# Optimization experiments

Measured on AMD Instinct MI355X. Metric: run time of the kernel, lower is better.

## Reference

```python
import jax, jax.numpy as jnp
import numpy as np

B, T, C, NH = 4, 2048, 1024, 16
HD = C // NH  # head dim = 64


def setup_inputs() -> dict:
    key = jax.random.key(0)
    ks = jax.random.split(key, 5)
    s = 0.02
    return {
        "x": jax.random.normal(ks[0], (B, T, C), dtype=jnp.float32),
        "W_attn": jax.random.normal(ks[1], (C, 3 * C), dtype=jnp.float32) * s,
        "b_attn": jnp.zeros((3 * C,), dtype=jnp.float32),
        "W_proj": jax.random.normal(ks[2], (C, C), dtype=jnp.float32) * s,
        "b_proj": jnp.zeros((C,), dtype=jnp.float32),
    }


def reference(x, W_attn, b_attn, W_proj, b_proj):
    Bv, Tv, Cv = x.shape
    qkv = x @ W_attn + b_attn  # [B,T,3C]
    q, k, v = jnp.split(qkv, 3, axis=2)
    # [B,T,C] -> [B,NH,T,HD]
    def heads(t):
        return t.reshape(Bv, Tv, NH, HD).transpose(0, 2, 1, 3)
    q, k, v = heads(q), heads(k), heads(v)
    scores = jnp.einsum("bhqd,bhkd->bhqk", q, k) / jnp.sqrt(jnp.float32(HD))
    causal = jnp.tril(jnp.ones((Tv, Tv), dtype=bool))
    scores = jnp.where(causal[None, None, :, :], scores, jnp.float32(-jnp.inf))
    probs = jax.nn.softmax(scores, axis=-1)
    # dropout rate is 0.0 -> identity
    y = jnp.einsum("bhqk,bhkd->bhqd", probs, v)
    y = y.transpose(0, 2, 1, 3).reshape(Bv, Tv, Cv)
    return y @ W_proj + b_proj
```

## Files before the change

kernel.cpp:

```cpp
#include <hip/hip_runtime.h>
#include <hip/hip_bf16.h>

#define Bsz 4
#define Tseq 2048
#define Cdim 1024
#define NH 16
#define HD 64
#define Mrows (Bsz*Tseq)
#define N3C (3*Cdim)

typedef __attribute__((ext_vector_type(8))) short short8;
typedef __attribute__((ext_vector_type(4))) short short4v;
typedef __attribute__((ext_vector_type(4))) float float4v;

__device__ __forceinline__ unsigned short f2b(float f) {
    union { float f; unsigned u; } x; x.f = f;
    unsigned u = x.u;
    u += 0x7fff + ((u >> 16) & 1);
    return (unsigned short)(u >> 16);
}

__device__ __forceinline__ unsigned pk2bf(float a, float b) {
#if __has_builtin(__builtin_amdgcn_cvt_pk_bf16_f32)
    auto w = __builtin_amdgcn_cvt_pk_bf16_f32(a, b);
    unsigned u; __builtin_memcpy(&u, &w, 4);
    return u;
#else
    return (unsigned)f2b(a) | ((unsigned)f2b(b) << 16);
#endif
}

#define GLDS(gp, lp) __builtin_amdgcn_global_load_lds(                         \
    (const __attribute__((address_space(1))) unsigned*)(gp),                   \
    (__attribute__((address_space(3))) unsigned*)(lp), 16, 0, 0)

__global__ __launch_bounds__(256) void cast_kernel(const float* __restrict__ in,
                                                   unsigned short* __restrict__ out, int n) {
    int i = (blockIdx.x * 256 + threadIdx.x) * 4;
    if (i < n) {
        float4 v = *reinterpret_cast<const float4*>(in + i);
        ushort4 o;
        o.x = f2b(v.x); o.y = f2b(v.y); o.z = f2b(v.z); o.w = f2b(v.w);
        *reinterpret_cast<ushort4*>(out + i) = o;
    }
}

__global__ __launch_bounds__(256) void transpose_cast(const float* __restrict__ in,
                                                      unsigned short* __restrict__ out,
                                                      int K, int N) {
    __shared__ float tile[32][33];
    int n0 = blockIdx.x * 32, k0 = blockIdx.y * 32;
    int tx = threadIdx.x & 31, ty = threadIdx.x >> 5;
    #pragma unroll
    for (int i = 0; i < 32; i += 8)
        tile[ty + i][tx] = in[(k0 + ty + i) * N + n0 + tx];
    __syncthreads();
    #pragma unroll
    for (int i = 0; i < 32; i += 8)
        out[(size_t)(n0 + ty + i) * K + k0 + tx] = f2b(tile[tx][ty + i]);
}


#define GROW(r) ((r) * 64 + ((r) >> 3) * 8)

template<bool QKV, int NCOL>
__global__ __launch_bounds__(256) void gemm_bt(const unsigned short* __restrict__ A,
                                               const unsigned short* __restrict__ Bt,
                                               const float* __restrict__ bias,
                                               unsigned short* __restrict__ qb,
                                               unsigned short* __restrict__ kb,
                                               unsigned short* __restrict__ vb,
                                               float* __restrict__ out) {
    __shared__ unsigned short As[8320];
    __shared__ unsigned short Bs[8320];
    int tid = threadIdx.x;
    int lane = tid & 63, wave = tid >> 6;
    int wm = wave >> 1, wn = wave & 1;
    int l15 = lane & 15, quad = lane >> 4;

    int f = blockIdx.x;
    int xcd = f & 7, slot = f >> 3;
    int rowblk = xcd * 8 + (slot & 7);
    int colblk = slot >> 3;
    int row0 = rowblk * 128;
    int col0 = colblk * 128;

    const unsigned short* Ag = A + (size_t)(row0 + wave * 32 + (lane >> 3)) * Cdim + (lane & 7) * 8;
    const unsigned short* Bg = Bt + (size_t)(col0 + wave * 32 + (lane >> 3)) * Cdim + (lane & 7) * 8;
    unsigned short* Al = &As[wave * 2080];
    unsigned short* Bl = &Bs[wave * 2080];

    float4v acc[4][4] = {};

    for (int k0 = 0; k0 < Cdim; k0 += 64) {
        __syncthreads();
        #pragma unroll
        for (int c = 0; c < 4; c++) {
            GLDS(Ag + k0 + (size_t)(c * 8) * Cdim, Al + c * 520);
            GLDS(Bg + k0 + (size_t)(c * 8) * Cdim, Bl + c * 520);
        }
        __syncthreads();

        #pragma unroll
        for (int g = 0; g < 2; g++) {
            short8 af[4], bf[4];
            #pragma unroll
            for (int mi = 0; mi < 4; mi++)
                af[mi] = *(const short8*)&As[GROW(wm * 64 + mi * 16 + l15) + g * 32 + quad * 8];
            #pragma unroll
            for (int ni = 0; ni < 4; ni++)
                bf[ni] = *(const short8*)&Bs[GROW(wn * 64 + ni * 16 + l15) + g * 32 + quad * 8];
            #pragma unroll
            for (int mi = 0; mi < 4; mi++)
                #pragma unroll
                for (int ni = 0; ni < 4; ni++)
                    acc[mi][ni] = __builtin_amdgcn_mfma_f32_16x16x32_bf16(af[mi], bf[ni], acc[mi][ni], 0, 0, 0);
        }
    }

    #pragma unroll
    for (int mi = 0; mi < 4; mi++) {
        #pragma unroll
        for (int ni = 0; ni < 4; ni++) {
            int colb = col0 + wn * 64 + ni * 16 + l15;
            int rowb = row0 + wm * 64 + mi * 16 + quad * 4;
            if (QKV) {
                int p = colb >> 10;
                int h = (colb & 1023) >> 6;
                int d = colb & 63;
                int b = rowb >> 11;
                int t = rowb & 2047;
                if (p == 2) {
                    ushort4 pk;
                    pk.x = f2b(acc[mi][ni][0] + bias[colb]);
                    pk.y = f2b(acc[mi][ni][1] + bias[colb]);
                    pk.z = f2b(acc[mi][ni][2] + bias[colb]);
                    pk.w = f2b(acc[mi][ni][3] + bias[colb]);
                    *(ushort4*)&vb[((size_t)(b * NH + h) * HD + d) * Tseq + t] = pk;
                } else {
                    unsigned short* dst = (p == 0) ? qb : kb;
                    #pragma unroll
                    for (int r = 0; r < 4; r++)
                        dst[((size_t)(b * NH + h) * Tseq + (t + r)) * HD + d] =
                            f2b(acc[mi][ni][r] + bias[colb]);
                }
            } else {
                #pragma unroll
                for (int r = 0; r < 4; r++)
                    out[(size_t)(rowb + r) * Cdim + colb] = acc[mi][ni][r] + bias[colb];
            }
        }
    }
}


__global__ __launch_bounds__(128, 3) void attn_kernel(const unsigned short* __restrict__ qb,
                                                      const unsigned short* __restrict__ kb,
                                                      const unsigned short* __restrict__ vt,
                                                      unsigned short* __restrict__ yb) {
    __shared__ unsigned short Ks[2][64 * 64];
    __shared__ unsigned short Vs[2][64 * 64];

    int tid = threadIdx.x;
    int lane = tid & 63, wave = tid >> 6;
    int l15 = lane & 15, quad = lane >> 4;
    int bh = blockIdx.x;
    int qt = 31 - blockIdx.y;

    const unsigned short* Qh = qb + (size_t)bh * Tseq * HD;
    const unsigned short* Kh = kb + (size_t)bh * Tseq * HD;
    const unsigned short* Vh = vt + (size_t)bh * HD * Tseq;
    int b = bh >> 4, h = bh & 15;
    const float cexp = 0.18033688011112042f;

    int q0 = qt * 64;
    int rb0 = q0 + wave * 32;

    short8 qf[2][2];
    #pragma unroll
    for (int mi = 0; mi < 2; mi++)
        #pragma unroll
        for (int g = 0; g < 2; g++)
            qf[mi][g] = *(const short8*)(Qh + (size_t)(rb0 + mi * 16 + l15) * HD + g * 32 + quad * 8);

    int srow = lane >> 3;
    int scol = ((lane & 7) ^ srow) * 8;
    int sx = l15 & 7;
    int kx0 = ((0 * 4 + quad) ^ sx) * 8;
    int kx1 = ((1 * 4 + quad) ^ sx) * 8;
    int qh_ = quad >> 1, ql_ = quad & 1;

    float4v ov[2][4] = {};
    float m[2]  = {-1e30f, -1e30f};
    float lp[2] = {0.f, 0.f};

    for (int j0 = 0; j0 <= q0; j0 += 128) {
        __syncthreads();
        {
            int jb = j0 + wave * 64;
            const unsigned short* Kg = Kh + (size_t)(jb + srow) * HD + scol;
            const unsigned short* Vg = Vh + (size_t)srow * Tseq + jb + scol;
            unsigned short* Kl = &Ks[wave][0];
            unsigned short* Vl = &Vs[wave][0];
            #pragma unroll
            for (int cc = 0; cc < 8; cc++) {
                GLDS(Kg + (size_t)(cc * 8) * HD, Kl + cc * 512);
                GLDS(Vg + (size_t)(cc * 8) * Tseq, Vl + cc * 512);
            }
        }
        __syncthreads();

        int nh = (j0 + 64 <= q0) ? 2 : 1;
        #pragma unroll 1
        for (int hh = 0; hh < nh; hh++) {
            int j0h = j0 + hh * 64;
            const unsigned short* Kl = &Ks[hh][0];
            const unsigned short* Vl = &Vs[hh][0];

            float4v st[2][4];
            #pragma unroll
            for (int mi = 0; mi < 2; mi++)
                #pragma unroll
                for (int kg = 0; kg < 4; kg++)
                    st[mi][kg] = (float4v){0.f, 0.f, 0.f, 0.f};
            #pragma unroll
            for (int kg = 0; kg < 4; kg++) {
                int krow = kg * 1024 + l15 * 64;
                short8 kf0 = *(const short8*)&Kl[krow + kx0];
                short8 kf1 = *(const short8*)&Kl[krow + kx1];
                st[0][kg] = __builtin_amdgcn_mfma_f32_16x16x32_bf16(kf0, qf[0][0], st[0][kg], 0, 0, 0);
                st[0][kg] = __builtin_amdgcn_mfma_f32_16x16x32_bf16(kf1, qf[0][1], st[0][kg], 0, 0, 0);
                st[1][kg] = __builtin_amdgcn_mfma_f32_16x16x32_bf16(kf0, qf[1][0], st[1][kg], 0, 0, 0);
                st[1][kg] = __builtin_amdgcn_mfma_f32_16x16x32_bf16(kf1, qf[1][1], st[1][kg], 0, 0, 0);
            }

            if (j0h == q0) {
                #pragma unroll
                for (int mi = 0; mi < 2; mi++) {
                    int qrow = rb0 + mi * 16 + l15;
                    #pragma unroll
                    for (int kg = 0; kg < 4; kg++) {
                        int keyb = j0h + kg * 16 + quad * 4;
                        #pragma unroll
                        for (int r = 0; r < 4; r++)
                            if (keyb + r > qrow) st[mi][kg][r] = -1e30f;
                    }
                }
            }

            short4v pf[2][4];
            #pragma unroll
            for (int mi = 0; mi < 2; mi++) {
                float mx = st[mi][0][0];
                #pragma unroll
                for (int kg = 0; kg < 4; kg++)
                    #pragma unroll
                    for (int r = 0; r < 4; r++)
                        mx = fmaxf(mx, st[mi][kg][r]);
                mx = fmaxf(mx, __shfl_xor(mx, 16));
                mx = fmaxf(mx, __shfl_xor(mx, 32));
                float mn = fmaxf(m[mi], mx);
                if (__any(mn > m[mi])) {
                    float alv = __builtin_amdgcn_exp2f((m[mi] - mn) * cexp);
                    m[mi] = mn;
                    lp[mi] *= alv;
                    float ar_[4];
                    #pragma unroll
                    for (int r = 0; r < 4; r++)
                        ar_[r] = __shfl(alv, quad * 4 + r);
                    #pragma unroll
                    for (int dg = 0; dg < 4; dg++)
                        #pragma unroll
                        for (int r = 0; r < 4; r++)
                            ov[mi][dg][r] *= ar_[r];
                }
                float mc = -m[mi] * cexp;
                float sum = 0.f;
                #pragma unroll
                for (int kg = 0; kg < 4; kg++) {
                    float p0 = __builtin_amdgcn_exp2f(__builtin_fmaf(st[mi][kg][0], cexp, mc));
                    float p1 = __builtin_amdgcn_exp2f(__builtin_fmaf(st[mi][kg][1], cexp, mc));
                    float p2 = __builtin_amdgcn_exp2f(__builtin_fmaf(st[mi][kg][2], cexp, mc));
                    float p3 = __builtin_amdgcn_exp2f(__builtin_fmaf(st[mi][kg][3], cexp, mc));
                    sum += (p0 + p1) + (p2 + p3);
                    union { unsigned u[2]; short4v s; } pk_;
                    pk_.u[0] = pk2bf(p0, p1);
                    pk_.u[1] = pk2bf(p2, p3);
                    pf[mi][kg] = pk_.s;
                }
                lp[mi] += sum;
            }

            #pragma unroll
            for (int kg = 0; kg < 4; kg++) {
                int vx = (((kg * 2 + qh_) ^ sx) << 3) + ql_ * 4;
                #pragma unroll
                for (int dg = 0; dg < 4; dg++) {
                    short4v vf = *(const short4v*)&Vl[dg * 1024 + l15 * 64 + vx];
                    ov[0][dg] = __builtin_amdgcn_mfma_f32_16x16x16bf16_1k(pf[0][kg], vf, ov[0][dg], 0, 0, 0);
                    ov[1][dg] = __builtin_amdgcn_mfma_f32_16x16x16bf16_1k(pf[1][kg], vf, ov[1][dg], 0, 0, 0);
                }
            }
        }
    }

    #pragma unroll
    for (int mi = 0; mi < 2; mi++) {
        float lf = lp[mi];
        lf += __shfl_xor(lf, 16);
        lf += __shfl_xor(lf, 32);
        float rinv[4];
        #pragma unroll
        for (int r = 0; r < 4; r++)
            rinv[r] = 1.0f / __shfl(lf, quad * 4 + r);
        #pragma unroll
        for (int dg = 0; dg < 4; dg++)
            #pragma unroll
            for (int r = 0; r < 4; r++) {
                int t = rb0 + mi * 16 + quad * 4 + r;
                yb[((size_t)b * Tseq + t) * Cdim + h * HD + dg * 16 + l15] =
                    f2b(ov[mi][dg][r] * rinv[r]);
            }
    }
}

extern "C" void kernel_launch(void* const* d_in, const int* in_sizes, int n_in,
                              void* d_out, int out_size, void* d_ws, size_t ws_size,
                              hipStream_t stream) {
    const float* x  = (const float*)d_in[0];
    const float* Wa = (const float*)d_in[1];
    const float* ba = (const float*)d_in[2];
    const float* Wp = (const float*)d_in[3];
    const float* bp = (const float*)d_in[4];
    float* out = (float*)d_out;

    unsigned short* ws = (unsigned short*)d_ws;
    unsigned short* xb  = ws;
    unsigned short* Wat = xb  + (size_t)Mrows * Cdim;
    unsigned short* Wpt = Wat + (size_t)N3C * Cdim;
    unsigned short* qb  = Wpt + (size_t)Cdim * Cdim;
    unsigned short* kb  = qb  + (size_t)Bsz * NH * Tseq * HD;
    unsigned short* vb  = kb  + (size_t)Bsz * NH * Tseq * HD;
    unsigned short* yb  = vb  + (size_t)Bsz * NH * Tseq * HD;

    int nx = Mrows * Cdim;
    cast_kernel<<<nx / 4 / 256, 256, 0, stream>>>(x, xb, nx);
    transpose_cast<<<dim3(N3C / 32, Cdim / 32), 256, 0, stream>>>(Wa, Wat, Cdim, N3C);
    transpose_cast<<<dim3(Cdim / 32, Cdim / 32), 256, 0, stream>>>(Wp, Wpt, Cdim, Cdim);

    gemm_bt<true, 24><<<64 * 24, 256, 0, stream>>>(
        xb, Wat, ba, qb, kb, vb, nullptr);

    attn_kernel<<<dim3(Bsz * NH, 32), 128, 0, stream>>>(qb, kb, vb, yb);

    gemm_bt<false, 8><<<64 * 8, 256, 0, stream>>>(
        yb, Wpt, bp, nullptr, nullptr, nullptr, out);
}
```

Measured before the change: 292.7 us.

## Restructure attention into 4-wave blocks with double-buffered K/V prefetch and lazy rescale

The attention kernel moves from 2-wave blocks handling 64 query rows to 4-wave blocks handling 128 query rows, so each K/V tile staged in LDS is shared by twice as many query rows. K/V loading becomes a double-buffered pipeline: the next 64-key tile is prefetched while the current one is computed, with one barrier per iteration. Waves skip key tiles lying fully beyond their causal range. Online-softmax rescaling now happens only when the running max grows by more than a threshold, which cuts rescale work but lets unnormalised exponentials reach larger magnitudes.

```diff
diff --git a/kernel.cpp b/kernel.cpp
--- a/kernel.cpp
+++ b/kernel.cpp
@@ -154,7 +154,7 @@
 }
 
 
-__global__ __launch_bounds__(128, 3) void attn_kernel(const unsigned short* __restrict__ qb,
+__global__ __launch_bounds__(256, 4) void attn_kernel(const unsigned short* __restrict__ qb,
                                                       const unsigned short* __restrict__ kb,
                                                       const unsigned short* __restrict__ vt,
                                                       unsigned short* __restrict__ yb) {
@@ -165,7 +165,7 @@
     int lane = tid & 63, wave = tid >> 6;
     int l15 = lane & 15, quad = lane >> 4;
     int bh = blockIdx.x;
-    int qt = 31 - blockIdx.y;
+    int qt = 15 - blockIdx.y;
 
     const unsigned short* Qh = qb + (size_t)bh * Tseq * HD;
     const unsigned short* Kh = kb + (size_t)bh * Tseq * HD;
@@ -173,7 +173,7 @@
     int b = bh >> 4, h = bh & 15;
     const float cexp = 0.18033688011112042f;
 
-    int q0 = qt * 64;
+    int q0 = qt * 128;
     int rb0 = q0 + wave * 32;
 
     short8 qf[2][2];
@@ -185,37 +185,45 @@
 
     int srow = lane >> 3;
     int scol = ((lane & 7) ^ srow) * 8;
+    const unsigned short* Kg0 = Kh + (size_t)(wave * 16 + srow) * HD + scol;
+    const unsigned short* Vg0 = Vh + (size_t)(wave * 16 + srow) * Tseq + scol;
+    unsigned short* Kl0 = &Ks[0][wave * 1024];
+    unsigned short* Vl0 = &Vs[0][wave * 1024];
+    unsigned short* Kl1 = &Ks[1][wave * 1024];
+    unsigned short* Vl1 = &Vs[1][wave * 1024];
+
     int sx = l15 & 7;
-    int kx0 = ((0 * 4 + quad) ^ sx) * 8;
-    int kx1 = ((1 * 4 + quad) ^ sx) * 8;
+    int kx0 = (quad ^ sx) * 8;
+    int kx1 = ((4 + quad) ^ sx) * 8;
     int qh_ = quad >> 1, ql_ = quad & 1;
 
     float4v ov[2][4] = {};
     float m[2]  = {-1e30f, -1e30f};
     float lp[2] = {0.f, 0.f};
 
-    for (int j0 = 0; j0 <= q0; j0 += 128) {
-        __syncthreads();
-        {
-            int jb = j0 + wave * 64;
-            const unsigned short* Kg = Kh + (size_t)(jb + srow) * HD + scol;
-            const unsigned short* Vg = Vh + (size_t)srow * Tseq + jb + scol;
-            unsigned short* Kl = &Ks[wave][0];
-            unsigned short* Vl = &Vs[wave][0];
-            #pragma unroll
-            for (int cc = 0; cc < 8; cc++) {
-                GLDS(Kg + (size_t)(cc * 8) * HD, Kl + cc * 512);
-                GLDS(Vg + (size_t)(cc * 8) * Tseq, Vl + cc * 512);
-            }
-        }
-        __syncthreads();
-
-        int nh = (j0 + 64 <= q0) ? 2 : 1;
-        #pragma unroll 1
-        for (int hh = 0; hh < nh; hh++) {
-            int j0h = j0 + hh * 64;
-            const unsigned short* Kl = &Ks[hh][0];
-            const unsigned short* Vl = &Vs[hh][0];
+    int nw = (q0 >> 6) + 2;
+
+    GLDS(Kg0, Kl0);                GLDS(Kg0 + 8 * HD, Kl0 + 512);
+    GLDS(Vg0, Vl0);                GLDS(Vg0 + 8 * Tseq, Vl0 + 512);
+    __syncthreads();
+
+    #pragma unroll 1
+    for (int it = 0; it < nw; ++it) {
+        int j0 = it << 6;
+
+        if (it + 1 < nw) {
+            int jn = j0 + 64;
+            unsigned short* Kl = (it & 1) ? Kl0 : Kl1;
+            unsigned short* Vl = (it & 1) ? Vl0 : Vl1;
+            GLDS(Kg0 + (size_t)jn * HD, Kl);
+            GLDS(Kg0 + (size_t)(jn + 8) * HD, Kl + 512);
+            GLDS(Vg0 + jn, Vl);
+            GLDS(Vg0 + 8 * Tseq + jn, Vl + 512);
+        }
+
+        if (j0 <= rb0 + 31) {
+            const unsigned short* Kl = &Ks[it & 1][0];
+            const unsigned short* Vl = &Vs[it & 1][0];
 
             float4v st[2][4];
             #pragma unroll
@@ -234,13 +242,13 @@
                 st[1][kg] = __builtin_amdgcn_mfma_f32_16x16x32_bf16(kf1, qf[1][1], st[1][kg], 0, 0, 0);
             }
 
-            if (j0h == q0) {
+            if (j0 + 63 > rb0) {
                 #pragma unroll
                 for (int mi = 0; mi < 2; mi++) {
                     int qrow = rb0 + mi * 16 + l15;
                     #pragma unroll
                     for (int kg = 0; kg < 4; kg++) {
-                        int keyb = j0h + kg * 16 + quad * 4;
+                        int keyb = j0 + kg * 16 + quad * 4;
                         #pragma unroll
                         for (int r = 0; r < 4; r++)
                             if (keyb + r > qrow) st[mi][kg][r] = -1e30f;
@@ -259,8 +267,8 @@
                         mx = fmaxf(mx, st[mi][kg][r]);
                 mx = fmaxf(mx, __shfl_xor(mx, 16));
                 mx = fmaxf(mx, __shfl_xor(mx, 32));
-                float mn = fmaxf(m[mi], mx);
-                if (__any(mn > m[mi])) {
+                if (__any(mx > m[mi] + 16.0f)) {
+                    float mn = fmaxf(m[mi], mx);
                     float alv = __builtin_amdgcn_exp2f((m[mi] - mn) * cexp);
                     m[mi] = mn;
                     lp[mi] *= alv;
@@ -302,6 +310,8 @@
                 }
             }
         }
+
+        __syncthreads();
     }
 
     #pragma unroll
@@ -351,7 +361,7 @@
     gemm_bt<true, 24><<<64 * 24, 256, 0, stream>>>(
         xb, Wat, ba, qb, kb, vb, nullptr);
 
-    attn_kernel<<<dim3(Bsz * NH, 32), 128, 0, stream>>>(qb, kb, vb, yb);
+    attn_kernel<<<dim3(Bsz * NH, 16), 256, 0, stream>>>(qb, kb, vb, yb);
 
     gemm_bt<false, 8><<<64 * 8, 256, 0, stream>>>(
         yb, Wpt, bp, nullptr, nullptr, nullptr, out);
```

After: 266.5 us. 1.1x faster.
